# Performance work log

Hardware: AMD Instinct MI355X
Metric: run time of the kernel (lower is better)

The kernel has to match this reference:

```python
import jax, jax.numpy as jnp
import numpy as np

EMB = 1024
HEADS = 16
HEAD_DIM = EMB // HEADS


def setup_inputs() -> dict:
    key = jax.random.key(0)
    ks = jax.random.split(key, 9)
    s = 1.0 / np.sqrt(EMB)
    x = jax.random.normal(ks[0], (4, 2048, EMB), dtype=jnp.float32)
    Wq = jax.random.uniform(ks[1], (EMB, EMB), minval=-s, maxval=s, dtype=jnp.float32)
    bq = jax.random.uniform(ks[2], (EMB,), minval=-s, maxval=s, dtype=jnp.float32)
    Wk = jax.random.uniform(ks[3], (EMB, EMB), minval=-s, maxval=s, dtype=jnp.float32)
    bk = jax.random.uniform(ks[4], (EMB,), minval=-s, maxval=s, dtype=jnp.float32)
    Wv = jax.random.uniform(ks[5], (EMB, EMB), minval=-s, maxval=s, dtype=jnp.float32)
    bv = jax.random.uniform(ks[6], (EMB,), minval=-s, maxval=s, dtype=jnp.float32)
    Wo = jax.random.uniform(ks[7], (EMB, EMB), minval=-s, maxval=s, dtype=jnp.float32)
    bo = jax.random.uniform(ks[8], (EMB,), minval=-s, maxval=s, dtype=jnp.float32)
    return {"x": x, "Wq": Wq, "bq": bq, "Wk": Wk, "bk": bk, "Wv": Wv, "bv": bv, "Wo": Wo, "bo": bo}


def reference(x, Wq, bq, Wk, bk, Wv, bv, Wo, bo):
    B, S, E = x.shape
    # QKV projections (torch Linear: y = x W^T + b)
    q = x @ Wq.T + bq
    k = x @ Wk.T + bk
    v = x @ Wv.T + bv
    # split heads -> [B, H, S, Dh]
    q = q.reshape(B, S, HEADS, HEAD_DIM).transpose(0, 2, 1, 3)
    k = k.reshape(B, S, HEADS, HEAD_DIM).transpose(0, 2, 1, 3)
    v = v.reshape(B, S, HEADS, HEAD_DIM).transpose(0, 2, 1, 3)
    # NOTE: module scales by 1/sqrt(emb_size), NOT 1/sqrt(head_dim)
    scale = 1.0 / jnp.sqrt(jnp.asarray(E, dtype=x.dtype))
    energy = jnp.einsum('bhqd,bhkd->bhqk', q, k) * scale
    attention = jax.nn.softmax(energy, axis=-1)
    out = jnp.einsum('bhqk,bhkd->bhqd', attention, v)
    out = out.transpose(0, 2, 1, 3).reshape(B, S, E)
    return out @ Wo.T + bo
```

## Files before the change

kernel.cpp:

```cpp
#include <hip/hip_runtime.h>


typedef __bf16 bf16;
typedef __attribute__((ext_vector_type(4))) short shortx4;
typedef __attribute__((ext_vector_type(8))) short short8;
typedef __attribute__((ext_vector_type(4))) float floatx4;
typedef __attribute__((ext_vector_type(2))) unsigned int uintx2;
typedef __attribute__((ext_vector_type(4))) unsigned int uintx4;

#define MFMA16(a, b, c) __builtin_amdgcn_mfma_f32_16x16x32_bf16((a), (b), (c), 0, 0, 0)

#define LDS_STRIDE 56

__device__ __forceinline__ float fast_exp2(float x) {
    float r;
    asm("v_exp_f32 %0, %1" : "=v"(r) : "v"(x));
    return r;
}
__device__ __forceinline__ unsigned int cvt_pk_bf16(float lo, float hi) {
    unsigned int r;
    asm("v_cvt_pk_bf16_f32 %0, %1, %2" : "=v"(r) : "v"(lo), "v"(hi));
    return r;
}

__device__ __forceinline__ void async16(const bf16* __restrict__ g, short* l) {
    __builtin_amdgcn_global_load_lds((const __attribute__((address_space(1))) void*)g,
                                     (__attribute__((address_space(3))) void*)l, 16, 0, 0);
}

__device__ __forceinline__ short8 frag8(const bf16* __restrict__ p) {
    return *(const short8*)p;
}
__device__ __forceinline__ short8 frag8(const float* __restrict__ p) {
    const floatx4 a = *(const floatx4*)p;
    const floatx4 b = *(const floatx4*)(p + 4);
    short8 r;
#pragma unroll
    for (int j = 0; j < 4; j++) {
        r[j]     = __builtin_bit_cast(short, (bf16)a[j]);
        r[4 + j] = __builtin_bit_cast(short, (bf16)b[j]);
    }
    return r;
}

__global__ __launch_bounds__(256) void to_bf16(
    const float* __restrict__ in, bf16* __restrict__ out, int n8)
{
    const int i = blockIdx.x * 256 + threadIdx.x;
    if (i >= n8) return;
    const floatx4 a = *(const floatx4*)(in + (size_t)i * 8);
    const floatx4 b = *(const floatx4*)(in + (size_t)i * 8 + 4);
    short8 r;
#pragma unroll
    for (int j = 0; j < 4; j++) {
        r[j]     = __builtin_bit_cast(short, (bf16)a[j]);
        r[4 + j] = __builtin_bit_cast(short, (bf16)b[j]);
    }
    *(short8*)((short*)out + (size_t)i * 8) = r;
}

__global__ __launch_bounds__(256) void to_bf16_w4(
    const float* __restrict__ Wq, const float* __restrict__ Wk,
    const float* __restrict__ Wv, const float* __restrict__ Wo,
    bf16* __restrict__ out)
{
    const int i = blockIdx.x * 256 + threadIdx.x;
    const int t = i >> 17;
    const int j = i & 131071;
    const float* src = (t == 0) ? Wq : (t == 1) ? Wk : (t == 2) ? Wv : Wo;
    const floatx4 a = *(const floatx4*)(src + (size_t)j * 8);
    const floatx4 b = *(const floatx4*)(src + (size_t)j * 8 + 4);
    short8 r;
#pragma unroll
    for (int jj = 0; jj < 4; jj++) {
        r[jj]     = __builtin_bit_cast(short, (bf16)a[jj]);
        r[4 + jj] = __builtin_bit_cast(short, (bf16)b[jj]);
    }
    *(short8*)((short*)out + (size_t)t * 1048576 + (size_t)j * 8) = r;
}

__device__ __forceinline__ void gemm128_db(
    const bf16* __restrict__ A, const bf16* __restrict__ B,
    int m0, int n0, short* As, short* Bs, floatx4 acc[4][4])
{
    const int tid  = threadIdx.x;
    const int lane = tid & 63;
    const int w    = tid >> 6;
    const int wu   = __builtin_amdgcn_readfirstlane(w);
    const int wm   = w >> 1, wn = w & 1;
    const int g    = lane >> 4, c = lane & 15;
    const int ar   = lane >> 2;
    const int aq   = ((lane & 3) ^ (ar & 3)) * 8;
    const int aswz = (g ^ (c & 3)) * 8;

#pragma unroll
    for (int mi = 0; mi < 4; mi++)
#pragma unroll
        for (int ni = 0; ni < 4; ni++)
            acc[mi][ni] = (floatx4){0.f, 0.f, 0.f, 0.f};

    const bf16* Arow0 = A + (size_t)(m0 + w * 32 + ar) * 1024 + aq;
    const bf16* Arow1 = A + (size_t)(m0 + w * 32 + 16 + ar) * 1024 + aq;
    const bf16* Brow0 = B + (size_t)(n0 + w * 32 + ar) * 1024 + aq;
    const bf16* Brow1 = B + (size_t)(n0 + w * 32 + 16 + ar) * 1024 + aq;

    async16(Arow0, As + wu * 1024);
    async16(Arow1, As + wu * 1024 + 512);
    async16(Brow0, Bs + wu * 1024);
    async16(Brow1, Bs + wu * 1024 + 512);
    __syncthreads();

    int cur = 0;
    for (int k0 = 0; k0 < 1024; k0 += 32) {
        if (k0 < 992) {
            const int kn = k0 + 32;
            short* Ad = As + (cur ^ 1) * 4096 + wu * 1024;
            short* Bd = Bs + (cur ^ 1) * 4096 + wu * 1024;
            async16(Arow0 + kn, Ad);
            async16(Arow1 + kn, Ad + 512);
            async16(Brow0 + kn, Bd);
            async16(Brow1 + kn, Bd + 512);
        }

        const short* Ac = As + cur * 4096;
        const short* Bc = Bs + cur * 4096;
        short8 af[4], bfr[4];
#pragma unroll
        for (int mi = 0; mi < 4; mi++)
            af[mi] = *(const short8*)(Ac + (wm * 64 + mi * 16 + c) * 32 + aswz);
#pragma unroll
        for (int ni = 0; ni < 4; ni++)
            bfr[ni] = *(const short8*)(Bc + (wn * 64 + ni * 16 + c) * 32 + aswz);
#pragma unroll
        for (int mi = 0; mi < 4; mi++)
#pragma unroll
            for (int ni = 0; ni < 4; ni++)
                acc[mi][ni] = MFMA16(af[mi], bfr[ni], acc[mi][ni]);

        if (k0 < 992) __syncthreads();
        cur ^= 1;
    }
}

__device__ __forceinline__ void gemm128_fallback(
    const bf16* __restrict__ A, const float* __restrict__ B,
    int m0, int n0, short* As, short* Bs, floatx4 acc[4][4])
{
    const int tid  = threadIdx.x;
    const int lane = tid & 63;
    const int w    = tid >> 6;
    const int wu   = __builtin_amdgcn_readfirstlane(w);
    const int wm   = w >> 1, wn = w & 1;
    const int g    = lane >> 4, c = lane & 15;
    const int ar = lane >> 2;
    const int aq = ((lane & 3) ^ (ar & 3)) * 8;
    const int lrow = tid >> 2;
    const int lc8  = (tid & 3) * 8;

#pragma unroll
    for (int mi = 0; mi < 4; mi++)
#pragma unroll
        for (int ni = 0; ni < 4; ni++)
            acc[mi][ni] = (floatx4){0.f, 0.f, 0.f, 0.f};

    const int aswz = (g ^ (c & 3)) * 8;

    for (int k0 = 0; k0 < 1024; k0 += 32) {
        async16(A + (size_t)(m0 + w * 32 + ar) * 1024 + k0 + aq,      As + wu * 1024);
        async16(A + (size_t)(m0 + w * 32 + 16 + ar) * 1024 + k0 + aq, As + wu * 1024 + 512);
        *(short8*)(Bs + lrow * LDS_STRIDE + lc8) =
            frag8(B + (size_t)(n0 + lrow) * 1024 + k0 + lc8);
        *(short8*)(Bs + (lrow + 64) * LDS_STRIDE + lc8) =
            frag8(B + (size_t)(n0 + lrow + 64) * 1024 + k0 + lc8);
        __syncthreads();

        short8 af[4], bfr[4];
#pragma unroll
        for (int mi = 0; mi < 4; mi++)
            af[mi] = *(const short8*)(As + (wm * 64 + mi * 16 + c) * 32 + aswz);
#pragma unroll
        for (int ni = 0; ni < 4; ni++)
            bfr[ni] = *(const short8*)(Bs + (wn * 64 + ni * 16 + c) * LDS_STRIDE + g * 8);
#pragma unroll
        for (int mi = 0; mi < 4; mi++)
#pragma unroll
            for (int ni = 0; ni < 4; ni++)
                acc[mi][ni] = MFMA16(af[mi], bfr[ni], acc[mi][ni]);
        __syncthreads();
    }
}

template <typename TB>
__global__ __launch_bounds__(256) void qkv_gemm(
    const bf16* __restrict__ Xb,
    const TB* __restrict__ Wq, const TB* __restrict__ Wk, const TB* __restrict__ Wv,
    const float* __restrict__ bq, const float* __restrict__ bk, const float* __restrict__ bv,
    bf16* __restrict__ qkv)
{
    __shared__ __align__(16) short As[(sizeof(TB) == 2) ? 8192 : 4096];
    __shared__ __align__(16) short Bs[(sizeof(TB) == 2) ? 8192 : 128 * LDS_STRIDE];

    const int z = blockIdx.z;
    const TB* W       = (z == 0) ? Wq : (z == 1) ? Wk : Wv;
    const float* bias = (z == 0) ? bq : (z == 1) ? bk : bv;
    bf16* outz = qkv + (size_t)z * (8192u * 1024u);

    const int m0 = blockIdx.y * 128;
    const int n0 = blockIdx.x * 128;

    floatx4 acc[4][4];
    if constexpr (sizeof(TB) == 2)
        gemm128_db(Xb, (const bf16*)W, m0, n0, As, Bs, acc);
    else
        gemm128_fallback(Xb, (const float*)W, m0, n0, As, Bs, acc);

    const int lane = threadIdx.x & 63;
    const int w = threadIdx.x >> 6;
    const int wm = w >> 1, wn = w & 1;
    const int g = lane >> 4, c = lane & 15;

    if (z == 2) {
#pragma unroll
        for (int ni = 0; ni < 4; ni++) {
            const int n = n0 + wn * 64 + ni * 16 + c;
            const float bb = bias[n];
            const int h = n >> 6, d = n & 63;
#pragma unroll
            for (int mi = 0; mi < 4; mi++) {
                const int m = m0 + wm * 64 + mi * 16 + g * 4;
                const int b = m >> 11, s = m & 2047;
                shortx4 st;
#pragma unroll
                for (int r = 0; r < 4; r++)
                    st[r] = __builtin_bit_cast(short, (bf16)(acc[mi][ni][r] + bb));
                *(shortx4*)&outz[(((size_t)((b << 4) | h)) * 64 + d) * 2048 + s] = st;
            }
        }
    } else {
#pragma unroll
        for (int ni = 0; ni < 4; ni++) {
            const int n = n0 + wn * 64 + ni * 16 + c;
            const float bb = bias[n];
            const int h = n >> 6, d = n & 63;
#pragma unroll
            for (int mi = 0; mi < 4; mi++) {
#pragma unroll
                for (int r = 0; r < 4; r++) {
                    const int m = m0 + wm * 64 + mi * 16 + g * 4 + r;
                    const int b = m >> 11, s = m & 2047;
                    outz[(((size_t)((b << 4) | h)) * 2048 + s) * 64 + d] =
                        (bf16)(acc[mi][ni][r] + bb);
                }
            }
        }
    }
}

__global__ __launch_bounds__(256, 2) void attn_kernel(
    const bf16* __restrict__ qkv, bf16* __restrict__ attn_out)
{
    __shared__ __align__(16) short Ks[2][128 * 64];
    __shared__ __align__(16) short Vs[2][64 * 128];

    const int linear = blockIdx.y * gridDim.x + blockIdx.x;
    const int slot = linear >> 3;
    const int bh = (linear & 7) * 8 + (slot >> 4);
    const int q0 = (slot & 15) * 128;

    const size_t HSTRIDE = 2048u * 64u;
    const bf16* __restrict__ Q  = qkv + (size_t)bh * HSTRIDE;
    const bf16* __restrict__ Kp = qkv + 8192u * 1024u + (size_t)bh * HSTRIDE;
    const bf16* __restrict__ Vt = qkv + 2u * 8192u * 1024u + (size_t)bh * HSTRIDE;

    const int tid  = threadIdx.x;
    const int lane = tid & 63;
    const int w    = tid >> 6;
    const int wu   = __builtin_amdgcn_readfirstlane(w);
    const int g    = lane >> 4, c = lane & 15;

    const float C2 = 0.04508422002778f;

    const int krow_off = lane >> 3;
    const int kchunk   = (lane & 7) ^ (lane >> 3);
    const int vrow_off = lane >> 4;

    short8 qf[2][2];
#pragma unroll
    for (int qb = 0; qb < 2; qb++)
#pragma unroll
        for (int ks = 0; ks < 2; ks++)
            qf[qb][ks] = *(const short8*)(Q + (size_t)(q0 + w * 32 + qb * 16 + c) * 64
                                            + ks * 32 + g * 8);

    floatx4 o[2][4];
#pragma unroll
    for (int mi = 0; mi < 2; mi++)
#pragma unroll
        for (int di = 0; di < 4; di++)
            o[mi][di] = (floatx4){0.f, 0.f, 0.f, 0.f};
    float m_run[2] = {-1e30f, -1e30f};
    float l_run[2] = {0.f, 0.f};

#pragma unroll
    for (int s = 0; s < 4; s++) {
        const int row = w * 32 + s * 8 + krow_off;
        async16(Kp + (size_t)row * 64 + kchunk * 8, &Ks[0][(wu * 32 + s * 8) * 64]);
    }
#pragma unroll
    for (int s = 0; s < 4; s++) {
        const int row = w * 16 + s * 4 + vrow_off;
        const int vchunk = (lane & 15) ^ (row & 15);
        async16(Vt + (size_t)row * 2048 + vchunk * 8, &Vs[0][(wu * 16 + s * 4) * 128]);
    }
    __syncthreads();

    int cur = 0;
    for (int kb = 0; kb < 16; kb++) {
        if (kb < 15) {
            const int kn = (kb + 1) * 128;
#pragma unroll
            for (int s = 0; s < 4; s++) {
                const int row = w * 32 + s * 8 + krow_off;
                async16(Kp + (size_t)(kn + row) * 64 + kchunk * 8,
                        &Ks[cur ^ 1][(wu * 32 + s * 8) * 64]);
            }
#pragma unroll
            for (int s = 0; s < 4; s++) {
                const int row = w * 16 + s * 4 + vrow_off;
                const int vchunk = (lane & 15) ^ (row & 15);
                async16(Vt + (size_t)row * 2048 + kn + vchunk * 8,
                        &Vs[cur ^ 1][(wu * 16 + s * 4) * 128]);
            }
        }

        const short* __restrict__ Kc = &Ks[cur][0];
        const short* __restrict__ Vc = &Vs[cur][0];

        floatx4 sAcc[2][8];
#pragma unroll
        for (int qb = 0; qb < 2; qb++)
#pragma unroll
            for (int ni = 0; ni < 8; ni++)
                sAcc[qb][ni] = (floatx4){0.f, 0.f, 0.f, 0.f};
#pragma unroll
        for (int ks = 0; ks < 2; ks++)
#pragma unroll
            for (int ni = 0; ni < 8; ni++) {
                const short8 kf = *(const short8*)(
                    Kc + (16 * ni + c) * 64 + (((ks * 4 + g) ^ (c & 7)) * 8));
                sAcc[0][ni] = MFMA16(kf, qf[0][ks], sAcc[0][ni]);
                sAcc[1][ni] = MFMA16(kf, qf[1][ks], sAcc[1][ni]);
            }

        float alpha[2];
        unsigned int lo[2][8], hi[2][8];
#pragma unroll
        for (int qb = 0; qb < 2; qb++) {
            floatx4 mv = sAcc[qb][0];
#pragma unroll
            for (int ni = 1; ni < 8; ni++)
#pragma unroll
                for (int r = 0; r < 4; r++) mv[r] = fmaxf(mv[r], sAcc[qb][ni][r]);
            float mx = fmaxf(fmaxf(mv[0], mv[1]), fmaxf(mv[2], mv[3]));
            mx = fmaxf(mx, __shfl_xor(mx, 16));
            mx = fmaxf(mx, __shfl_xor(mx, 32));
            const float mnew = fmaxf(m_run[qb], mx * C2);
            alpha[qb] = fast_exp2(m_run[qb] - mnew);
            m_run[qb] = mnew;

            floatx4 sv = {0.f, 0.f, 0.f, 0.f};
#pragma unroll
            for (int ni = 0; ni < 8; ni++) {
#pragma unroll
                for (int r = 0; r < 4; r++) {
                    const float p = fast_exp2(fmaf(sAcc[qb][ni][r], C2, -mnew));
                    sAcc[qb][ni][r] = p;
                    sv[r] += p;
                }
                lo[qb][ni] = cvt_pk_bf16(sAcc[qb][ni][0], sAcc[qb][ni][1]);
                hi[qb][ni] = cvt_pk_bf16(sAcc[qb][ni][2], sAcc[qb][ni][3]);
            }
            float sum = (sv[0] + sv[1]) + (sv[2] + sv[3]);
            sum += __shfl_xor(sum, 16);
            sum += __shfl_xor(sum, 32);
            l_run[qb] = l_run[qb] * alpha[qb] + sum;
        }

#pragma unroll
        for (int mi = 0; mi < 2; mi++)
#pragma unroll
            for (int r = 0; r < 4; r++) {
                const int src = (lane & 48) | (g * 4 + r);
                const float a = __shfl(alpha[mi], src);
#pragma unroll
                for (int di = 0; di < 4; di++) o[mi][di][r] *= a;
            }

#pragma unroll
        for (int t = 0; t < 4; t++) {
            const short8 pf0 = __builtin_bit_cast(short8,
                (uintx4){lo[0][2 * t], hi[0][2 * t], lo[0][2 * t + 1], hi[0][2 * t + 1]});
            const short8 pf1 = __builtin_bit_cast(short8,
                (uintx4){lo[1][2 * t], hi[1][2 * t], lo[1][2 * t + 1], hi[1][2 * t + 1]});
#pragma unroll
            for (int di = 0; di < 4; di++) {
                const int rowb = (16 * di + c) * 128 + 4 * (g & 1);
                const uintx2 vlo = *(const uintx2*)(
                    Vc + rowb + (((4 * t + (g >> 1)) ^ c) * 8));
                const uintx2 vhi = *(const uintx2*)(
                    Vc + rowb + (((4 * t + 2 + (g >> 1)) ^ c) * 8));
                const short8 vf = __builtin_bit_cast(short8,
                    (uintx4){vlo[0], vlo[1], vhi[0], vhi[1]});
                o[0][di] = MFMA16(pf0, vf, o[0][di]);
                o[1][di] = MFMA16(pf1, vf, o[1][di]);
            }
        }

        if (kb < 15) __syncthreads();
        cur ^= 1;
    }

    const int b = bh >> 4, h = bh & 15;
#pragma unroll
    for (int mi = 0; mi < 2; mi++) {
#pragma unroll
        for (int r = 0; r < 4; r++) {
            const int src = (lane & 48) | (g * 4 + r);
            const float linv = 1.0f / __shfl(l_run[mi], src);
            const int srow = q0 + w * 32 + mi * 16 + g * 4 + r;
#pragma unroll
            for (int di = 0; di < 4; di++) {
                attn_out[((size_t)(b * 2048 + srow)) * 1024 + h * 64 + di * 16 + c] =
                    (bf16)(o[mi][di][r] * linv);
            }
        }
    }
}

template <typename TB>
__global__ __launch_bounds__(256) void out_gemm(
    const bf16* __restrict__ A, const TB* __restrict__ Wo,
    const float* __restrict__ bo, float* __restrict__ C)
{
    __shared__ __align__(16) short As[(sizeof(TB) == 2) ? 8192 : 4096];
    __shared__ __align__(16) short Bs[(sizeof(TB) == 2) ? 8192 : 128 * LDS_STRIDE];

    const int m0 = blockIdx.y * 128;
    const int n0 = blockIdx.x * 128;

    floatx4 acc[4][4];
    if constexpr (sizeof(TB) == 2)
        gemm128_db(A, (const bf16*)Wo, m0, n0, As, Bs, acc);
    else
        gemm128_fallback(A, (const float*)Wo, m0, n0, As, Bs, acc);

    const int lane = threadIdx.x & 63;
    const int w = threadIdx.x >> 6;
    const int wm = w >> 1, wn = w & 1;
    const int g = lane >> 4, c = lane & 15;

#pragma unroll
    for (int ni = 0; ni < 4; ni++) {
        const int n = n0 + wn * 64 + ni * 16 + c;
        const float bb = bo[n];
#pragma unroll
        for (int mi = 0; mi < 4; mi++) {
#pragma unroll
            for (int r = 0; r < 4; r++) {
                const int m = m0 + wm * 64 + mi * 16 + g * 4 + r;
                C[(size_t)m * 1024 + n] = acc[mi][ni][r] + bb;
            }
        }
    }
}

extern "C" void kernel_launch(void* const* d_in, const int* in_sizes, int n_in,
                              void* d_out, int out_size, void* d_ws, size_t ws_size,
                              hipStream_t stream)
{
    const float* x  = (const float*)d_in[0];
    const float* Wq = (const float*)d_in[1];
    const float* bq = (const float*)d_in[2];
    const float* Wk = (const float*)d_in[3];
    const float* bk = (const float*)d_in[4];
    const float* Wv = (const float*)d_in[5];
    const float* bv = (const float*)d_in[6];
    const float* Wo = (const float*)d_in[7];
    const float* bo = (const float*)d_in[8];
    float* out = (float*)d_out;

    bf16* qkv  = (bf16*)d_ws;
    bf16* attn = qkv + 3u * 8192u * 1024u;
    bf16* xb   = attn;

    const size_t base = 64u * 1024u * 1024u;
    const bool haveW = ws_size >= base + 8u * 1024u * 1024u;
    bf16* wb = (bf16*)((char*)d_ws + base);

    to_bf16<<<dim3(4096), dim3(256), 0, stream>>>(x, xb, 1048576);

    if (haveW) {
        to_bf16_w4<<<dim3(2048), dim3(256), 0, stream>>>(Wq, Wk, Wv, Wo, wb);
        qkv_gemm<bf16><<<dim3(8, 64, 3), dim3(256), 0, stream>>>(
            xb, wb, wb + 1048576u, wb + 2u * 1048576u, bq, bk, bv, qkv);
    } else {
        qkv_gemm<float><<<dim3(8, 64, 3), dim3(256), 0, stream>>>(
            xb, Wq, Wk, Wv, bq, bk, bv, qkv);
    }

    attn_kernel<<<dim3(16, 64), dim3(256), 0, stream>>>(qkv, attn);

    if (haveW) {
        out_gemm<bf16><<<dim3(8, 64), dim3(256), 0, stream>>>(
            attn, wb + 3u * 1048576u, bo, out);
    } else {
        out_gemm<float><<<dim3(8, 64), dim3(256), 0, stream>>>(attn, Wo, bo, out);
    }
}
```

Before: 343.1 us.

## Switch GEMM mainloop to triple-buffered async LDS pipeline with one barrier

Replaces the double-buffered GEMM mainloop used by the QKV and output projections with a three-stage ring of LDS buffers. Two K-tiles are prefetched ahead, and the loop waits on vmcnt counts instead of full syncthreads, so each iteration needs only one barrier. Global loads now get more time to overlap MFMA work. In exchange, LDS per block grows by half, which may lower occupancy, and correctness depends on the hand-written waitcnt accounting.

```diff
diff --git a/kernel.cpp b/kernel.cpp
--- a/kernel.cpp
+++ b/kernel.cpp
@@ -79,7 +79,7 @@
     *(short8*)((short*)out + (size_t)t * 1048576 + (size_t)j * 8) = r;
 }
 
-__device__ __forceinline__ void gemm128_db(
+__device__ __forceinline__ void gemm128_p3(
     const bf16* __restrict__ A, const bf16* __restrict__ B,
     int m0, int n0, short* As, short* Bs, floatx4 acc[4][4])
 {
@@ -104,23 +104,22 @@
     const bf16* Brow0 = B + (size_t)(n0 + w * 32 + ar) * 1024 + aq;
     const bf16* Brow1 = B + (size_t)(n0 + w * 32 + 16 + ar) * 1024 + aq;
 
-    async16(Arow0, As + wu * 1024);
-    async16(Arow1, As + wu * 1024 + 512);
-    async16(Brow0, Bs + wu * 1024);
-    async16(Brow1, Bs + wu * 1024 + 512);
-    __syncthreads();
+    {
+        short* Ad = As + wu * 1024;
+        short* Bd = Bs + wu * 1024;
+        async16(Arow0, Ad);        async16(Arow1, Ad + 512);
+        async16(Brow0, Bd);        async16(Brow1, Bd + 512);
+        async16(Arow0 + 32, Ad + 4096);  async16(Arow1 + 32, Ad + 4096 + 512);
+        async16(Brow0 + 32, Bd + 4096);  async16(Brow1 + 32, Bd + 4096 + 512);
+    }
 
     int cur = 0;
-    for (int k0 = 0; k0 < 1024; k0 += 32) {
-        if (k0 < 992) {
-            const int kn = k0 + 32;
-            short* Ad = As + (cur ^ 1) * 4096 + wu * 1024;
-            short* Bd = Bs + (cur ^ 1) * 4096 + wu * 1024;
-            async16(Arow0 + kn, Ad);
-            async16(Arow1 + kn, Ad + 512);
-            async16(Brow0 + kn, Bd);
-            async16(Brow1 + kn, Bd + 512);
-        }
+    for (int t = 0; t < 32; ++t) {
+        if (t < 31) asm volatile("s_waitcnt vmcnt(4)" ::: "memory");
+        else        asm volatile("s_waitcnt vmcnt(0)" ::: "memory");
+        __builtin_amdgcn_sched_barrier(0);
+        __builtin_amdgcn_s_barrier();
+        __builtin_amdgcn_sched_barrier(0);
 
         const short* Ac = As + cur * 4096;
         const short* Bc = Bs + cur * 4096;
@@ -137,8 +136,15 @@
             for (int ni = 0; ni < 4; ni++)
                 acc[mi][ni] = MFMA16(af[mi], bfr[ni], acc[mi][ni]);
 
-        if (k0 < 992) __syncthreads();
-        cur ^= 1;
+        if (t < 30) {
+            const int kn  = (t + 2) * 32;
+            const int nb  = (cur == 0) ? 2 : cur - 1;
+            short* Ad = As + nb * 4096 + wu * 1024;
+            short* Bd = Bs + nb * 4096 + wu * 1024;
+            async16(Arow0 + kn, Ad);   async16(Arow1 + kn, Ad + 512);
+            async16(Brow0 + kn, Bd);   async16(Brow1 + kn, Bd + 512);
+        }
+        cur = (cur == 2) ? 0 : cur + 1;
     }
 }
 
@@ -197,8 +203,8 @@
     const float* __restrict__ bq, const float* __restrict__ bk, const float* __restrict__ bv,
     bf16* __restrict__ qkv)
 {
-    __shared__ __align__(16) short As[(sizeof(TB) == 2) ? 8192 : 4096];
-    __shared__ __align__(16) short Bs[(sizeof(TB) == 2) ? 8192 : 128 * LDS_STRIDE];
+    __shared__ __align__(16) short As[(sizeof(TB) == 2) ? 12288 : 4096];
+    __shared__ __align__(16) short Bs[(sizeof(TB) == 2) ? 12288 : 128 * LDS_STRIDE];
 
     const int z = blockIdx.z;
     const TB* W       = (z == 0) ? Wq : (z == 1) ? Wk : Wv;
@@ -210,7 +216,7 @@
 
     floatx4 acc[4][4];
     if constexpr (sizeof(TB) == 2)
-        gemm128_db(Xb, (const bf16*)W, m0, n0, As, Bs, acc);
+        gemm128_p3(Xb, (const bf16*)W, m0, n0, As, Bs, acc);
     else
         gemm128_fallback(Xb, (const float*)W, m0, n0, As, Bs, acc);
 
@@ -442,15 +448,15 @@
     const bf16* __restrict__ A, const TB* __restrict__ Wo,
     const float* __restrict__ bo, float* __restrict__ C)
 {
-    __shared__ __align__(16) short As[(sizeof(TB) == 2) ? 8192 : 4096];
-    __shared__ __align__(16) short Bs[(sizeof(TB) == 2) ? 8192 : 128 * LDS_STRIDE];
+    __shared__ __align__(16) short As[(sizeof(TB) == 2) ? 12288 : 4096];
+    __shared__ __align__(16) short Bs[(sizeof(TB) == 2) ? 12288 : 128 * LDS_STRIDE];
 
     const int m0 = blockIdx.y * 128;
     const int n0 = blockIdx.x * 128;
 
     floatx4 acc[4][4];
     if constexpr (sizeof(TB) == 2)
-        gemm128_db(A, (const bf16*)Wo, m0, n0, As, Bs, acc);
+        gemm128_p3(A, (const bf16*)Wo, m0, n0, As, Bs, acc);
     else
         gemm128_fallback(A, (const float*)Wo, m0, n0, As, Bs, acc);
 
```

New measurement: 321.0 us. -6.4%, faster.
